# Kernel tuning notes

Hardware: AMD Instinct MI355X
Metric: run time of the kernel (lower is better)

The kernel has to match this reference:

```python
import jax, jax.numpy as jnp
import numpy as np

NH = 16        # hidden buckets
NG = 32        # static attrs
NR = 16        # routing lags
HS = 256       # MLP hidden size
RHO_WARMUP = 639


def _mlp(x, W1, b1, W2, b2):
    # eval mode: dropout disabled
    return jnp.tanh(x @ W1 + b1) @ W2 + b2


def setup_inputs() -> dict:
    key = jax.random.key(0)
    ks = jax.random.split(key, 16)
    nt, ns = 1000, 500
    x = jax.random.normal(ks[0], (nt, ns, 6), dtype=jnp.float32)
    xc = jax.random.normal(ks[1], (ns, NG), dtype=jnp.float32)

    def lin(k, fan_in, fan_out):
        kw, kb = jax.random.split(k)
        s = 1.0 / np.sqrt(fan_in)
        W = jax.random.uniform(kw, (fan_in, fan_out), jnp.float32, -s, s)
        b = jax.random.uniform(kb, (fan_out,), jnp.float32, -s, s)
        return W, b

    Wr1, br1 = lin(ks[2], NG, HS)
    Wr2, br2 = lin(ks[3], HS, NH * NR)
    Ww1, bw1 = lin(ks[4], NG, HS)
    Ww2, bw2 = lin(ks[5], HS, NH * 7)
    Wt1, bt1 = lin(ks[6], 6 + NG, HS)
    Wt2, bt2 = lin(ks[7], HS, NH * 3)
    return dict(x=x, xc=xc, Wr1=Wr1, br1=br1, Wr2=Wr2, br2=br2,
                Ww1=Ww1, bw1=bw1, Ww2=Ww2, bw2=bw2,
                Wt1=Wt1, bt1=bt1, Wt2=Wt2, bt2=bt2)


def _forward(x, xc, Wr1, br1, Wr2, br2, Ww1, bw1, Ww2, bw2, Wt1, bt1, Wt2, bt2):
    nt, ns, _ = x.shape
    Prcp, Evp, T1, T2 = x[..., 0], x[..., 1], x[..., 2], x[..., 3]

    # ---- static per-basin gate params (wLst activations) ----
    w = _mlp(xc, Ww1, bw1, Ww2, bw2).reshape(ns, NH, 7)
    kp = jax.nn.sigmoid(w[..., 0])   # shallow fast outflow coef
    ksf = jax.nn.sigmoid(w[..., 1])  # shallow slow outflow coef
    kg = jax.nn.sigmoid(w[..., 2])   # deep outflow coef
    gr = jax.nn.sigmoid(w[..., 3])   # recharge fraction
    gL = jnp.exp(w[..., 4])          # shallow capacity
    qb = jax.nn.relu(w[..., 5])      # baseflow
    ga = jax.nn.softmax(w[..., 6], axis=-1)  # bucket mixture ('skip')

    # ---- time-varying params (vLst activations) ----
    xt = jnp.concatenate([x, jnp.broadcast_to(xc[None], (nt, ns, NG))], axis=-1)
    v = _mlp(xt, Wt1, bt1, Wt2, bt2).reshape(nt, ns, NH, 3)
    fi = jax.nn.sigmoid(v[..., 0])             # infiltration fraction
    fm = jax.nn.relu(v[..., 1])                # melt capacity
    Ev = Evp[..., None] * jnp.exp(v[..., 2])   # per-bucket ET

    # ---- divide precipitation into snow / liquid by temperature ----
    vp = jax.nn.sigmoid((T1 + T2) * 0.5)       # [nt, ns]
    Ps = (Prcp * (1.0 - vp))[..., None]        # snow   [nt, ns, 1]
    Pl = (Prcp * vp)[..., None]                # liquid [nt, ns, 1]

    # ---- fused bucket recurrence over time (single scan) ----
    def step(carry, inp):
        Sf, Ss, Sd = carry
        ps, pl, fi_t, fm_t, ev_t = inp
        # snow bucket (long)
        S1 = Sf + ps
        qf = jnp.minimum(S1, fm_t)
        Sf = S1 - qf
        # shallow bucket
        S2 = jax.nn.relu(Ss + pl * fi_t + qf - ev_t)
        qp = jax.nn.relu(S2 - gL) * kp
        qs = jnp.minimum(S2, gL) * ksf
        Ss = S2 - qp - qs
        # deep bucket
        S3 = Sd + qs * gr
        qd = S3 * kg + qb
        Sd = jax.nn.relu(S3 - qd)
        q = qp + qs * (1.0 - gr) + qd
        return (Sf, Ss, Sd), q

    z = jnp.zeros((ns, NH), dtype=x.dtype)
    _, Q = jax.lax.scan(step, (z, z, z), (Ps, Pl, fi, fm, Ev))  # Q: [nt, ns, NH]

    # ---- unit-hydrograph routing over NR lags ----
    r = jax.nn.softmax(_mlp(xc, Wr1, br1, Wr2, br2).reshape(ns, NH, NR), axis=-1)
    Qpad = jnp.pad(Q, ((NR - 1, 0), (0, 0), (0, 0)))
    yR = sum(Qpad[NR - 1 - j: NR - 1 - j + nt] * r[None, :, :, j] for j in range(NR))
    out = jnp.einsum('tsh,sh->ts', yR, ga)
    return out[RHO_WARMUP:]  # [nt - rho_warmup, ns]


def reference(x, xc, Wr1, br1, Wr2, br2, Ww1, bw1, Ww2, bw2, Wt1, bt1, Wt2, bt2):
    return _forward(x, xc, Wr1, br1, Wr2, br2, Ww1, bw1, Ww2, bw2, Wt1, bt1, Wt2, bt2)
```

## Files before the change

kernel.cpp:

```cpp
#include <hip/hip_runtime.h>
#include <hip/hip_fp16.h>

typedef __attribute__((ext_vector_type(8))) _Float16 half8;
typedef __attribute__((ext_vector_type(2))) _Float16 h2v;
typedef __attribute__((ext_vector_type(4))) float f32x4;
typedef __attribute__((ext_vector_type(4))) unsigned short u16x4;
typedef __attribute__((ext_vector_type(2))) unsigned int u32x2;
typedef __attribute__((ext_vector_type(4))) unsigned int u32x4;

#define NTT 1000
#define NSB 500
#define WARM 639
#define MKF (-2.8853900817779268f)

__device__ __forceinline__ float fsig(float x) {
  return __builtin_amdgcn_rcpf(1.f + __expf(-x));
}
__device__ __forceinline__ float ftanh(float x) {
  float e = __expf(-2.f * x);
  return fmaf(2.f, __builtin_amdgcn_rcpf(1.f + e), -1.f);
}
__device__ __forceinline__ __half2 u2h(unsigned int u) {
  __half2 h; *(unsigned int*)&h = u; return h;
}
__device__ __forceinline__ unsigned int h2u(__half2 h) {
  return *(unsigned int*)&h;
}
__device__ __forceinline__ __half2 hmin2(__half2 a, __half2 b) {
  h2v av = *(h2v*)&a, bv = *(h2v*)&b;
  h2v r = __builtin_elementwise_min(av, bv);
  return *(__half2*)&r;
}

__global__ __launch_bounds__(256) void static_kernel(
    const float* __restrict__ xc,
    const float* __restrict__ Wr1, const float* __restrict__ br1,
    const float* __restrict__ Wr2, const float* __restrict__ br2,
    const float* __restrict__ Ww1, const float* __restrict__ bw1,
    const float* __restrict__ Ww2, const float* __restrict__ bw2,
    const float* __restrict__ Wt1, const float* __restrict__ bt1,
    const float* __restrict__ Wt2, const float* __restrict__ bt2,
    _Float16* __restrict__ c_gh, float* __restrict__ params,
    float* __restrict__ rg,
    _Float16* __restrict__ BT, _Float16* __restrict__ W1h,
    float* __restrict__ bS)
{
  int s = blockIdx.x, tid = threadIdx.x;
  __shared__ float xcs[32];
  __shared__ float hw[256], hr[256];
  __shared__ float wout[112], rout[256];
  if (tid < 32) xcs[tid] = xc[s * 32 + tid];
  __syncthreads();
  {
    float aw = bw1[tid], ar = br1[tid], ac = bt1[tid];
    #pragma unroll 8
    for (int g = 0; g < 32; ++g) {
      float v = xcs[g];
      aw = fmaf(v, Ww1[g * 256 + tid], aw);
      ar = fmaf(v, Wr1[g * 256 + tid], ar);
      ac = fmaf(v, Wt1[(6 + g) * 256 + tid], ac);
    }
    hw[tid] = ftanh(aw);
    hr[tid] = ftanh(ar);
    c_gh[s * 256 + tid] = (_Float16)(ac * MKF);
  }
  __syncthreads();
  {
    float acc = br2[tid];
    #pragma unroll 8
    for (int k = 0; k < 256; ++k) acc = fmaf(hr[k], Wr2[k * 256 + tid], acc);
    rout[tid] = acc;
  }
  if (tid < 112) {
    float acc = bw2[tid];
    #pragma unroll 8
    for (int k = 0; k < 256; ++k) acc = fmaf(hw[k], Ww2[k * 112 + tid], acc);
    wout[tid] = acc;
  }
  __syncthreads();
  if (tid < 16) {
    int h = tid;
    float* P = params + (s * 16 + h) * 6;
    P[0] = fsig(wout[h * 7 + 0]);
    P[1] = fsig(wout[h * 7 + 1]);
    P[2] = fsig(wout[h * 7 + 2]);
    P[3] = fsig(wout[h * 7 + 3]);
    P[4] = __expf(wout[h * 7 + 4]);
    P[5] = fmaxf(wout[h * 7 + 5], 0.f);
    float m = -1e30f;
    for (int k = 0; k < 16; ++k) m = fmaxf(m, wout[k * 7 + 6]);
    float den = 0.f;
    for (int k = 0; k < 16; ++k) den += __expf(wout[k * 7 + 6] - m);
    float ga = __expf(wout[h * 7 + 6] - m) * __builtin_amdgcn_rcpf(den);
    float rm = -1e30f;
    for (int j = 0; j < 16; ++j) rm = fmaxf(rm, rout[h * 16 + j]);
    float rden = 0.f;
    for (int j = 0; j < 16; ++j) rden += __expf(rout[h * 16 + j] - rm);
    float sc = ga * __builtin_amdgcn_rcpf(rden);
    for (int j = 0; j < 16; ++j)
      rg[(s * 16 + h) * 16 + j] = __expf(rout[h * 16 + j] - rm) * sc;
  }
  if (s < 48) {
    int o = s, k = tid;
    float w2v = Wt2[k * 48 + o];
    int byte = o * 512 + ((k * 2) ^ ((o & 7) << 4));
    *(_Float16*)((char*)BT + byte) = (_Float16)w2v;
    if (s < 6) W1h[s * 256 + tid] = (_Float16)(Wt1[s * 256 + tid] * MKF);
    __syncthreads();
    hw[tid] = w2v;
    __syncthreads();
    for (int st = 128; st > 0; st >>= 1) {
      if (tid < st) hw[tid] += hw[tid + st];
      __syncthreads();
    }
    if (tid == 0) bS[o] = bt2[o] - hw[0];
  }
}

__global__ __launch_bounds__(256, 5) void tv_kernel(
    const float* __restrict__ x, const _Float16* __restrict__ W1h,
    const float* __restrict__ bS, const _Float16* __restrict__ c_gh,
    const _Float16* __restrict__ BTg,
    unsigned short* __restrict__ recP, int s_base)
{
  int s = blockIdx.x + s_base;
  int t0 = blockIdx.y * 64;
  int tid = threadIdx.x;
  int w = tid >> 6, l = tid & 63;

  __shared__ _Float16 Abuf[4][16][128];
  __shared__ _Float16 Bbuf[48 * 128];
  __shared__ __half2  xl2[64][8];
  __shared__ float    xe[64][4];

  for (int i = tid; i < 768; i += 256) {
    int o = i >> 4, j = i & 15;
    *(half8*)((char*)Bbuf + o * 256 + j * 16) =
        *(const half8*)((const char*)BTg + o * 512 + j * 16);
  }
  if (tid < 64) {
    int t = t0 + tid;
    float2 a = {0.f, 0.f}, b = a, c = a;
    if (t < NTT) {
      const float* xp = &x[((size_t)t * NSB + s) * 6];
      a = *(const float2*)(xp + 0);
      b = *(const float2*)(xp + 2);
      c = *(const float2*)(xp + 4);
    }
    float vp = fsig(0.5f * (b.x + b.y));
    xe[tid][0] = a.x * vp;
    xe[tid][1] = a.y;
    xe[tid][2] = a.x * (1.f - vp);
    xe[tid][3] = 0.f;
    xl2[tid][0] = __floats2half2_rn(a.x, a.x);
    xl2[tid][1] = __floats2half2_rn(a.y, a.y);
    xl2[tid][2] = __floats2half2_rn(b.x, b.x);
    xl2[tid][3] = __floats2half2_rn(b.y, b.y);
    xl2[tid][4] = __floats2half2_rn(c.x, c.x);
    xl2[tid][5] = __floats2half2_rn(c.y, c.y);
    xl2[tid][6] = __floats2half2_rn(0.f, 0.f);
    xl2[tid][7] = __floats2half2_rn(0.f, 0.f);
  }
  __syncthreads();

  const __half2 one2 = __floats2half2_rn(1.f, 1.f);
  const __half2 hi2  = __floats2half2_rn(15.5f, 15.5f);

  __half2 wlo[6], whi[6];
  #pragma unroll
  for (int c = 0; c < 6; ++c) {
    wlo[c] = *(const __half2*)&W1h[c * 256 + 2 * l];
    whi[c] = *(const __half2*)&W1h[c * 256 + 128 + 2 * l];
  }
  __half2 cglo = *(const __half2*)&c_gh[s * 256 + 2 * l];
  __half2 cghi = *(const __half2*)&c_gh[s * 256 + 128 + 2 * l];

  char* aw_base = (char*)&Abuf[w][0][0];
  int col = l & 15, q = l >> 4;
  int arow_xor = (col & 7) << 4;
  const char* Bb = (const char*)Bbuf;
  int r0 = 0 + col, r1 = 16 + col, r2 = 32 + col;
  f32x4 acc0 = {0.f, 0.f, 0.f, 0.f}, acc1 = acc0, acc2 = acc0;

  #pragma unroll
  for (int half = 0; half < 2; ++half) {
    if (half == 1) {
      __syncthreads();
      for (int i = tid; i < 768; i += 256) {
        int o = i >> 4, j = i & 15;
        *(half8*)((char*)Bbuf + o * 256 + j * 16) =
            *(const half8*)((const char*)BTg + o * 512 + 256 + j * 16);
      }
      __syncthreads();
    }
    const __half2* wv = half ? whi : wlo;
    __half2 cg2 = half ? cghi : cglo;
    #pragma unroll
    for (int tt = 0; tt < 16; ++tt) {
      int tr = w * 16 + tt;
      uint4 xa = *(const uint4*)&xl2[tr][0];
      uint2 xb = *(const uint2*)&xl2[tr][4];
      __half2 acc = cg2;
      acc = __hfma2(u2h(xa.x), wv[0], acc);
      acc = __hfma2(u2h(xa.y), wv[1], acc);
      acc = __hfma2(u2h(xa.z), wv[2], acc);
      acc = __hfma2(u2h(xa.w), wv[3], acc);
      acc = __hfma2(u2h(xb.x), wv[4], acc);
      acc = __hfma2(u2h(xb.y), wv[5], acc);
      __half2 e = h2exp2(hmin2(acc, hi2));
      __half2 sg = h2rcp(__hadd2(one2, e));
      int byte = tt * 256 + ((4 * l) ^ ((tt & 7) << 4));
      *(unsigned int*)(aw_base + byte) = h2u(sg);
    }
    #pragma unroll
    for (int ks = 0; ks < 4; ++ks) {
      int kof = ks * 64 + q * 16;
      half8 a  = *(const half8*)(aw_base + col * 256 + (kof ^ arow_xor));
      half8 b0 = *(const half8*)(Bb + r0 * 256 + (kof ^ ((r0 & 7) << 4)));
      half8 b1 = *(const half8*)(Bb + r1 * 256 + (kof ^ ((r1 & 7) << 4)));
      half8 b2 = *(const half8*)(Bb + r2 * 256 + (kof ^ ((r2 & 7) << 4)));
      acc0 = __builtin_amdgcn_mfma_f32_16x16x32_f16(a, b0, acc0, 0, 0, 0);
      acc1 = __builtin_amdgcn_mfma_f32_16x16x32_f16(a, b1, acc1, 0, 0, 0);
      acc2 = __builtin_amdgcn_mfma_f32_16x16x32_f16(a, b2, acc2, 0, 0, 0);
    }
  }

  float bs0 = bS[col], bs1 = bS[16 + col], bs2 = bS[32 + col];
  int c3 = col % 3;
  int ob0 = (3 - c3) % 3;
  int ob1 = (ob0 + 1) % 3;
  int ob2 = (ob0 + 2) % 3;
  int h0 = (16 * ob0 + col) / 3;
  int h1 = (16 * ob1 + col) / 3;
  int h2 = (16 * ob2 + col) / 3;
  #pragma unroll
  for (int i = 0; i < 4; ++i) {
    int tt = q * 4 + i;
    int t = t0 + w * 16 + tt;
    if (t >= NTT) continue;
    float2 pe = *(const float2*)&xe[w * 16 + tt][0];
    float vv0 = fmaf(2.f, acc0[i], bs0);
    float vv1 = fmaf(2.f, acc1[i], bs1);
    float vv2 = fmaf(2.f, acc2[i], bs2);
    float s0 = (ob0 == 0) ? vv0 : (ob0 == 1) ? vv1 : vv2;
    float s1 = (ob1 == 0) ? vv0 : (ob1 == 1) ? vv1 : vv2;
    float s2 = (ob2 == 0) ? vv0 : (ob2 == 1) ? vv1 : vv2;
    char* rowp = aw_base + tt * 128;
    *(__half*)(rowp + h0 * 8 + 0) = __float2half(pe.x * fsig(s0));
    *(__half*)(rowp + h1 * 8 + 2) = __float2half(fmaxf(s1, 0.f));
    *(__half*)(rowp + h2 * 8 + 4) = __float2half(pe.y * __expf(s2));
  }
  #pragma unroll
  for (int k2 = 0; k2 < 4; ++k2) {
    int idx = k2 * 64 + l;
    int tt = idx >> 4, h = idx & 15;
    int t = t0 + w * 16 + tt;
    if (t < NTT) {
      u16x4 r4 = *(const u16x4*)(aw_base + tt * 128 + h * 8);
      __half psh = __float2half(xe[w * 16 + tt][2]);
      r4[3] = *(unsigned short*)&psh;
      *(u16x4*)&recP[((size_t)t * 8000 + s * 16 + h) * 4] = r4;
    }
  }
}

struct Rec8 { u32x2 r[8]; };

__device__ __forceinline__ void issue8(Rec8& c, int tB, unsigned voff,
                                       const char* recP)
{
  #pragma unroll
  for (int u = 0; u < 8; ++u) {
    const char* base = recP + (size_t)(tB + u) * 64000;
    asm volatile("global_load_dwordx2 %0, %1, %2 offset:0"
                 : "=v"(c.r[u]) : "v"(voff), "s"(base));
  }
}

__device__ __forceinline__ void comp8(
    const Rec8& c, int tb, u32x4* Qlds4, int lane,
    float& Sf, float& Ss, float& Sd,
    float kp, float ksf, float kg, float gr, float gL, float qb, float omgr,
    float A0, float A1, float B1)
{
  float qv[8];
  #pragma unroll
  for (int u = 0; u < 8; ++u) {
    float2 pf = __half22float2(u2h(c.r[u].x));
    float2 ep = __half22float2(u2h(c.r[u].y));
    float ce    = pf.x - ep.x;
    float psmfm = ep.y - pf.y;
    float S1 = Sf + ep.y;
    float qf = fminf(S1, pf.y);
    Sf = fmaxf(Sf + psmfm, 0.f);
    float S2 = fmaxf((Ss + ce) + qf, 0.f);
    float qp = fmaxf(S2 - gL, 0.f) * kp;
    float qs = fminf(S2, gL) * ksf;
    bool le = S2 <= gL;
    Ss = fmaf(S2, le ? A0 : A1, le ? 0.f : B1);
    float S3 = fmaf(qs, gr, Sd);
    float qd = fmaf(S3, kg, qb);
    Sd = fmaxf(S3 - qd, 0.f);
    qv[u] = fmaf(qs, omgr, qp) + qd;
  }
  if (tb < NTT) {
    u32x4 q4;
    q4.x = h2u(__floats2half2_rn(qv[0], qv[1]));
    q4.y = h2u(__floats2half2_rn(qv[2], qv[3]));
    q4.z = h2u(__floats2half2_rn(qv[4], qv[5]));
    q4.w = h2u(__floats2half2_rn(qv[6], qv[7]));
    Qlds4[(tb >> 3) * 64 + lane] = q4;
  }
}

#define SCAN_PHASE(CK, OFF) \
  asm volatile("s_waitcnt vmcnt(40)" ::: "memory"); \
  __builtin_amdgcn_sched_barrier(0); \
  comp8(CK, tb + OFF, Qlds4, lane, Sf, Ss, Sd, kp, ksf, kg, gr, gL, qb, omgr, \
        A0, A1, B1); \
  issue8(CK, tb + 48 + OFF, voff, rb); \
  __builtin_amdgcn_sched_barrier(0);

__global__ __launch_bounds__(64, 1) void scan_kernel(
    const float* __restrict__ params,
    const unsigned short* __restrict__ recP,
    __half* __restrict__ Qg2)
{
  __shared__ u32x4 Qlds4[125 * 64];
  int lane = threadIdx.x;
  int tid = blockIdx.x * 64 + lane;
  unsigned voff = (unsigned)tid * 8;
  const float* P = params + tid * 6;
  float kp = P[0], ksf = P[1], kg = P[2], gr = P[3], gL = P[4], qb = P[5];
  float omgr = 1.f - gr;
  float A0 = 1.f - ksf, A1 = 1.f - kp, B1 = gL * (kp - ksf);
  asm volatile("" : "+v"(kp), "+v"(ksf), "+v"(kg), "+v"(gr), "+v"(gL));
  asm volatile("" : "+v"(qb), "+v"(omgr), "+v"(A0), "+v"(A1), "+v"(B1));
  asm volatile("s_waitcnt vmcnt(0)" ::: "memory");
  __builtin_amdgcn_sched_barrier(0);

  float Sf = 0.f, Ss = 0.f, Sd = 0.f;
  const char* rb = (const char*)recP;

  Rec8 C0, C1, C2, C3, C4, C5;
  issue8(C0,  0, voff, rb);
  issue8(C1,  8, voff, rb);
  issue8(C2, 16, voff, rb);
  issue8(C3, 24, voff, rb);
  issue8(C4, 32, voff, rb);
  issue8(C5, 40, voff, rb);
  __builtin_amdgcn_sched_barrier(0);
  for (int i = 0; i < 21; ++i) {
    int tb = i * 48;
    SCAN_PHASE(C0,  0)
    SCAN_PHASE(C1,  8)
    SCAN_PHASE(C2, 16)
    SCAN_PHASE(C3, 24)
    SCAN_PHASE(C4, 32)
    SCAN_PHASE(C5, 40)
  }
  asm volatile("s_waitcnt vmcnt(0)" ::: "memory");
  __builtin_amdgcn_sched_barrier(0);
  size_t gbase = (size_t)tid * 1024;
  for (int k = 0; k < 125; ++k) {
    u32x4 v = Qlds4[k * 64 + lane];
    *(u32x4*)(Qg2 + gbase + k * 8) = v;
  }
}

__global__ __launch_bounds__(128) void route_kernel(
    const __half* __restrict__ Qg2, const float* __restrict__ rg,
    float* __restrict__ out)
{
  int s = blockIdx.x;
  int t0 = WARM + blockIdx.y * 128;
  int tid = threadIdx.x;
  __shared__ float Qs[16][145];
  __shared__ float rgs[16][16];
  {
    int h = tid & 15, c = tid >> 4;
    const __half* src = Qg2 + (size_t)(s * 16 + h) * 1024 + (t0 - 15);
    #pragma unroll
    for (int cc = 0; cc < 3; ++cc) {
      int ch = c + cc * 8;
      if (ch < 18) {
        half8 v8 = *(const half8*)(src + ch * 8);
        #pragma unroll
        for (int j = 0; j < 8; ++j) {
          int idx = ch * 8 + j;
          if (idx < 143) Qs[h][idx] = (float)v8[j];
        }
      }
    }
  }
  for (int i = tid; i < 256; i += 128) {
    int h = i >> 4, j = i & 15;
    rgs[j][h] = rg[s * 256 + i];
  }
  __syncthreads();
  int t = t0 + tid;
  if (t < NTT) {
    float acc = 0.f;
    #pragma unroll
    for (int j = 0; j < 16; ++j) {
      int row = tid + 15 - j;
      #pragma unroll
      for (int h = 0; h < 16; ++h)
        acc = fmaf(Qs[h][row], rgs[j][h], acc);
    }
    out[(t - WARM) * NSB + s] = acc;
  }
}

extern "C" void kernel_launch(void* const* d_in, const int* in_sizes, int n_in,
                              void* d_out, int out_size, void* d_ws, size_t ws_size,
                              hipStream_t stream)
{
  const float* x   = (const float*)d_in[0];
  const float* xc  = (const float*)d_in[1];
  const float* Wr1 = (const float*)d_in[2];
  const float* br1 = (const float*)d_in[3];
  const float* Wr2 = (const float*)d_in[4];
  const float* br2 = (const float*)d_in[5];
  const float* Ww1 = (const float*)d_in[6];
  const float* bw1 = (const float*)d_in[7];
  const float* Ww2 = (const float*)d_in[8];
  const float* bw2 = (const float*)d_in[9];
  const float* Wt1 = (const float*)d_in[10];
  const float* bt1 = (const float*)d_in[11];
  const float* Wt2 = (const float*)d_in[12];
  const float* bt2 = (const float*)d_in[13];

  char* w = (char*)d_ws;
  unsigned short* recP = (unsigned short*)(w);
  __half* Qg2   = (__half*)(w + 64000000);
  float*  params= (float*)(w + 80384000);
  float*  rgw   = (float*)(w + 80576000);
  _Float16* BT  = (_Float16*)(w + 81088000);
  _Float16* W1h = (_Float16*)(w + 81112576);
  _Float16* c_gh= (_Float16*)(w + 81115648);
  float*  bS    = (float*)(w + 81371648);

  static_kernel<<<500, 256, 0, stream>>>(xc, Wr1, br1, Wr2, br2,
                                         Ww1, bw1, Ww2, bw2, Wt1, bt1,
                                         Wt2, bt2,
                                         c_gh, params, rgw, BT, W1h, bS);
  tv_kernel<<<dim3(250, 16), 256, 0, stream>>>(x, W1h, bS, c_gh, BT, recP, 0);
  tv_kernel<<<dim3(250, 16), 256, 0, stream>>>(x, W1h, bS, c_gh, BT, recP, 250);
  scan_kernel<<<125, 64, 0, stream>>>(params, recP, Qg2);
  route_kernel<<<dim3(500, 3), 128, 0, stream>>>(Qg2, rgw, (float*)d_out);
}
```

Baseline: 171.4 us.

## Interleave recP by 8-step time groups so scan loads use dwordx4

The intermediate per-timestep record buffer is re-laid out so that 8 consecutive timesteps for one (basin, bucket) sit contiguously in 64 bytes. The scan kernel can then fetch each 8-step chunk with four 16-byte loads instead of eight strided 8-byte loads, with the vmcnt wait threshold adjusted to match. The two half-grid tv_kernel launches are also merged into one launch over all basins. The tv_kernel writes now scatter with a 64-byte stride per (s,h), which may reduce write coalescing in the producer.

Result: faster. 160.2 us (-6.5%).

```diff
diff --git a/kernel.cpp b/kernel.cpp
--- a/kernel.cpp
+++ b/kernel.cpp
@@ -121,9 +121,9 @@
     const float* __restrict__ x, const _Float16* __restrict__ W1h,
     const float* __restrict__ bS, const _Float16* __restrict__ c_gh,
     const _Float16* __restrict__ BTg,
-    unsigned short* __restrict__ recP, int s_base)
-{
-  int s = blockIdx.x + s_base;
+    char* __restrict__ recP)
+{
+  int s = blockIdx.x;
   int t0 = blockIdx.y * 64;
   int tid = threadIdx.x;
   int w = tid >> 6, l = tid & 63;
@@ -259,22 +259,27 @@
       u16x4 r4 = *(const u16x4*)(aw_base + tt * 128 + h * 8);
       __half psh = __float2half(xe[w * 16 + tt][2]);
       r4[3] = *(unsigned short*)&psh;
-      *(u16x4*)&recP[((size_t)t * 8000 + s * 16 + h) * 4] = r4;
-    }
-  }
-}
-
-struct Rec8 { u32x2 r[8]; };
-
-__device__ __forceinline__ void issue8(Rec8& c, int tB, unsigned voff,
+      size_t off = ((size_t)(t >> 3) * 8000 + s * 16 + h) * 64
+                 + (size_t)(t & 7) * 8;
+      *(u16x4*)(recP + off) = r4;
+    }
+  }
+}
+
+struct Rec8 { u32x4 r[4]; };
+
+__device__ __forceinline__ void issue4(Rec8& c, int tB, unsigned voff,
                                        const char* recP)
 {
-  #pragma unroll
-  for (int u = 0; u < 8; ++u) {
-    const char* base = recP + (size_t)(tB + u) * 64000;
-    asm volatile("global_load_dwordx2 %0, %1, %2 offset:0"
-                 : "=v"(c.r[u]) : "v"(voff), "s"(base));
-  }
+  const char* base = recP + (size_t)(tB >> 3) * 512000;
+  asm volatile("global_load_dwordx4 %0, %1, %2 offset:0"
+               : "=v"(c.r[0]) : "v"(voff), "s"(base));
+  asm volatile("global_load_dwordx4 %0, %1, %2 offset:16"
+               : "=v"(c.r[1]) : "v"(voff), "s"(base));
+  asm volatile("global_load_dwordx4 %0, %1, %2 offset:32"
+               : "=v"(c.r[2]) : "v"(voff), "s"(base));
+  asm volatile("global_load_dwordx4 %0, %1, %2 offset:48"
+               : "=v"(c.r[3]) : "v"(voff), "s"(base));
 }
 
 __device__ __forceinline__ void comp8(
@@ -286,8 +291,10 @@
   float qv[8];
   #pragma unroll
   for (int u = 0; u < 8; ++u) {
-    float2 pf = __half22float2(u2h(c.r[u].x));
-    float2 ep = __half22float2(u2h(c.r[u].y));
+    unsigned rx = c.r[u >> 1][(u & 1) * 2];
+    unsigned ry = c.r[u >> 1][(u & 1) * 2 + 1];
+    float2 pf = __half22float2(u2h(rx));
+    float2 ep = __half22float2(u2h(ry));
     float ce    = pf.x - ep.x;
     float psmfm = ep.y - pf.y;
     float S1 = Sf + ep.y;
@@ -314,22 +321,22 @@
 }
 
 #define SCAN_PHASE(CK, OFF) \
-  asm volatile("s_waitcnt vmcnt(40)" ::: "memory"); \
+  asm volatile("s_waitcnt vmcnt(20)" ::: "memory"); \
   __builtin_amdgcn_sched_barrier(0); \
   comp8(CK, tb + OFF, Qlds4, lane, Sf, Ss, Sd, kp, ksf, kg, gr, gL, qb, omgr, \
         A0, A1, B1); \
-  issue8(CK, tb + 48 + OFF, voff, rb); \
+  issue4(CK, tb + 48 + OFF, voff, rb); \
   __builtin_amdgcn_sched_barrier(0);
 
 __global__ __launch_bounds__(64, 1) void scan_kernel(
     const float* __restrict__ params,
-    const unsigned short* __restrict__ recP,
+    const char* __restrict__ recP,
     __half* __restrict__ Qg2)
 {
   __shared__ u32x4 Qlds4[125 * 64];
   int lane = threadIdx.x;
   int tid = blockIdx.x * 64 + lane;
-  unsigned voff = (unsigned)tid * 8;
+  unsigned voff = (unsigned)tid * 64;
   const float* P = params + tid * 6;
   float kp = P[0], ksf = P[1], kg = P[2], gr = P[3], gL = P[4], qb = P[5];
   float omgr = 1.f - gr;
@@ -340,15 +347,15 @@
   __builtin_amdgcn_sched_barrier(0);
 
   float Sf = 0.f, Ss = 0.f, Sd = 0.f;
-  const char* rb = (const char*)recP;
+  const char* rb = recP;
 
   Rec8 C0, C1, C2, C3, C4, C5;
-  issue8(C0,  0, voff, rb);
-  issue8(C1,  8, voff, rb);
-  issue8(C2, 16, voff, rb);
-  issue8(C3, 24, voff, rb);
-  issue8(C4, 32, voff, rb);
-  issue8(C5, 40, voff, rb);
+  issue4(C0,  0, voff, rb);
+  issue4(C1,  8, voff, rb);
+  issue4(C2, 16, voff, rb);
+  issue4(C3, 24, voff, rb);
+  issue4(C4, 32, voff, rb);
+  issue4(C5, 40, voff, rb);
   __builtin_amdgcn_sched_barrier(0);
   for (int i = 0; i < 21; ++i) {
     int tb = i * 48;
@@ -432,7 +439,7 @@
   const float* bt2 = (const float*)d_in[13];
 
   char* w = (char*)d_ws;
-  unsigned short* recP = (unsigned short*)(w);
+  char*   recP  = w;
   __half* Qg2   = (__half*)(w + 64000000);
   float*  params= (float*)(w + 80384000);
   float*  rgw   = (float*)(w + 80576000);
@@ -445,8 +452,7 @@
                                          Ww1, bw1, Ww2, bw2, Wt1, bt1,
                                          Wt2, bt2,
                                          c_gh, params, rgw, BT, W1h, bS);
-  tv_kernel<<<dim3(250, 16), 256, 0, stream>>>(x, W1h, bS, c_gh, BT, recP, 0);
-  tv_kernel<<<dim3(250, 16), 256, 0, stream>>>(x, W1h, bS, c_gh, BT, recP, 250);
+  tv_kernel<<<dim3(500, 16), 256, 0, stream>>>(x, W1h, bS, c_gh, BT, recP);
   scan_kernel<<<125, 64, 0, stream>>>(params, recP, Qg2);
   route_kernel<<<dim3(500, 3), 128, 0, stream>>>(Qg2, rgw, (float*)d_out);
 }
```
